# Performance work log

Measured on AMD Instinct MI355X. Metric: run time of the kernel, lower is better.

## Reference

```python
import jax, jax.numpy as jnp
import numpy as np

B, N = 4096, 64
K1, K2, K3 = 32, 16, 8   # ceil(0.5 * n) at each SAGPooling stage
VOCAB, EMB, H = 25, 32, 128
IN = EMB + 2

def _init(k, shape, scale=None):
    if scale is None:
        scale = (2.0 / sum(shape)) ** 0.5
    return (jax.random.normal(k, shape) * scale).astype(jnp.float32)

def setup_inputs() -> dict:
    key = jax.random.key(0)
    ks = jax.random.split(key, 20)
    # band adjacency: residues within sequence distance 2 (peptide backbone graph)
    i = np.arange(N)
    band = ((np.abs(i[:, None] - i[None, :]) <= 2) & (i[:, None] != i[None, :])).astype(np.float32)
    adj = jnp.broadcast_to(jnp.asarray(band), (B, N, N))
    return dict(
        aa=jax.random.randint(ks[0], (B, N), 0, VOCAB),
        pos=jax.random.uniform(ks[1], (B, N, 1), dtype=jnp.float32),
        is_cdr3=(jax.random.uniform(ks[2], (B, N, 1)) < 0.3).astype(jnp.float32),
        adj=adj,
        emb=_init(ks[3], (VOCAB, EMB), 1.0),
        W1=_init(ks[4], (IN, H)), b1=jnp.zeros((H,), jnp.float32),
        p1_wl=_init(ks[5], (H, 1)), p1_bl=jnp.zeros((1,), jnp.float32), p1_wr=_init(ks[6], (H, 1)),
        W2=_init(ks[7], (H, H)), b2=jnp.zeros((H,), jnp.float32),
        p2_wl=_init(ks[8], (H, 1)), p2_bl=jnp.zeros((1,), jnp.float32), p2_wr=_init(ks[9], (H, 1)),
        W3=_init(ks[10], (H, H)), b3=jnp.zeros((H,), jnp.float32),
        p3_wl=_init(ks[11], (H, 1)), p3_bl=jnp.zeros((1,), jnp.float32), p3_wr=_init(ks[12], (H, 1)),
        mW1=_init(ks[13], (2 * H, H)), mb1=jnp.zeros((H,), jnp.float32),
        mW2=_init(ks[14], (H, H // 2)), mb2=jnp.zeros((H // 2,), jnp.float32),
        mW3=_init(ks[15], (H // 2, 1)), mb3=jnp.zeros((1,), jnp.float32),
    )

def _gcn(x, adj, W, b):
    # GCNConv: D^-1/2 (A+I) D^-1/2 (x W) + b
    n = adj.shape[-1]
    a = adj + jnp.eye(n, dtype=adj.dtype)
    dinv = jax.lax.rsqrt(jnp.maximum(a.sum(-1), 1e-12))
    norm = dinv[:, :, None] * a * dinv[:, None, :]
    return jnp.einsum('bij,bjf->bif', norm, x @ W) + b

def _sag_pool(x, adj, wl, bl, wr, k):
    # SAGPooling default GNN is GraphConv: score = W_rel (A x) + b + W_root x
    s = (jnp.einsum('bij,bjf->bif', adj, x) @ wl + bl + x @ wr)[..., 0]  # [B,n]
    vals, idx = jax.lax.top_k(s, k)                                      # per-graph top-k
    xs = jnp.take_along_axis(x, idx[:, :, None], axis=1) * jnp.tanh(vals)[:, :, None]
    a = jnp.take_along_axis(adj, idx[:, :, None], axis=1)                # filter edges to
    a = jnp.take_along_axis(a, idx[:, None, :], axis=2)                  # selected nodes
    return xs, a

def _readout(x):
    # cat([global_max_pool, global_mean_pool]) over nodes of each graph
    return jnp.concatenate([x.max(axis=1), x.mean(axis=1)], axis=-1)

def _forward(pos, is_cdr3, adj, emb, W1, b1, p1_wl, p1_bl, p1_wr, W2, b2, p2_wl, p2_bl, p2_wr, W3, b3, p3_wl, p3_bl, p3_wr, mW1, mb1, mW2, mb2, mW3, mb3, aa):
    x = jnp.concatenate([emb[aa], pos, is_cdr3], axis=-1)   # [B,N,IN]
    x = jax.nn.relu(_gcn(x, adj, W1, b1))
    x, a = _sag_pool(x, adj, p1_wl, p1_bl, p1_wr, K1)
    r = _readout(x)
    x = jax.nn.relu(_gcn(x, a, W2, b2))
    x, a = _sag_pool(x, a, p2_wl, p2_bl, p2_wr, K2)
    r = r + _readout(x)
    x = jax.nn.relu(_gcn(x, a, W3, b3))
    x, a = _sag_pool(x, a, p3_wl, p3_bl, p3_wr, K3)
    r = r + _readout(x)
    h = jax.nn.relu(r @ mW1 + mb1)   # dropout: identity in eval mode
    h = jax.nn.relu(h @ mW2 + mb2)
    return (h @ mW3 + mb3)[:, 0]     # logits [B]

def reference(aa, pos, is_cdr3, adj, emb, W1, b1, p1_wl, p1_bl, p1_wr, W2, b2, p2_wl, p2_bl, p2_wr, W3, b3, p3_wl, p3_bl, p3_wr, mW1, mb1, mW2, mb2, mW3, mb3):
    return _forward(pos, is_cdr3, adj, emb, W1, b1, p1_wl, p1_bl, p1_wr, W2, b2, p2_wl, p2_bl, p2_wr, W3, b3, p3_wl, p3_bl, p3_wr, mW1, mb1, mW2, mb2, mW3, mb3, aa)
```

## Files before the change

### kernel.cpp

```cpp
#include <hip/hip_runtime.h>
#include <math.h>

#define TPB 256
static constexpr int N0 = 64;
static constexpr int H  = 128;
static constexpr int LD = 132;

#define SCHED_FENCE() __builtin_amdgcn_sched_barrier(0)

typedef const __attribute__((address_space(1))) unsigned int glb_u32;
typedef __attribute__((address_space(3))) unsigned int lds_u32;

struct alignas(16) Shm {
  float B[32 * LD];
  float B2[2304];
  float dinvS[32];
  unsigned long long adjS[32];
};

__device__ __forceinline__ unsigned long long& adjPad(float* Bb, int i) {
  return *((unsigned long long*)(Bb + (i >> 1) * LD + 128) + (i & 1));
}

template<int W>
__device__ __forceinline__ float redsum(float v) {
  #pragma unroll
  for (int m = W >> 1; m; m >>= 1) v += __shfl_xor(v, m, 64);
  return v;
}
template<int W>
__device__ __forceinline__ int redsum_i(int v) {
  #pragma unroll
  for (int m = W >> 1; m; m >>= 1) v += __shfl_xor(v, m, 64);
  return v;
}

template<int NN, int GROUPS, int CPT, int STRIDE, bool PADJ>
__device__ __forceinline__ void agg_inplace(float* buf, float* adjb,
    const float* dinv, int tid) {
  float acc[CPT];
  const int i = tid & (NN - 1);
  const int g = tid / NN;
  const bool act = (g < GROUPS);
  if (act) {
    unsigned long long m =
        (PADJ ? adjPad(adjb, i) : ((const unsigned long long*)adjb)[i]) | (1ull << i);
    #pragma unroll
    for (int c = 0; c < CPT; ++c) acc[c] = 0.f;
    const float* base = buf + g * CPT;
    #pragma unroll 1
    while (m) {
      int j = __builtin_ctzll(m); m &= m - 1;
      float a = dinv[j];
      const float* xp = base + j * STRIDE;
      #pragma unroll
      for (int c = 0; c < CPT; c += 4) {
        float4 xv = *(const float4*)(xp + c);
        acc[c]     += a * xv.x; acc[c + 1] += a * xv.y;
        acc[c + 2] += a * xv.z; acc[c + 3] += a * xv.w;
      }
    }
    float di = dinv[i];
    #pragma unroll
    for (int c = 0; c < CPT; ++c) acc[c] *= di;
  }
  __syncthreads();
  if (act) {
    float* op = buf + i * STRIDE + g * CPT;
    #pragma unroll
    for (int c = 0; c < CPT; c += 4)
      *(float4*)(op + c) = make_float4(acc[c], acc[c + 1], acc[c + 2], acc[c + 3]);
  }
  __syncthreads();
  SCHED_FENCE();
}

template<int R, int K, int KREAL, int MODE>
__device__ __forceinline__ void gemm_gw(const float* z, int zld,
    const float* __restrict__ Wg, const float* __restrict__ bg,
    float* out, int old_,
    const float* __restrict__ wl, const float* __restrict__ wr,
    float* uuP, float* svP, const float* tvP, const int* selP, int tid) {
  constexpr int NR = R / 8;
  constexpr int KC = 4;
  const int fc = (tid & 31) * 4;
  const int r0 = (tid >> 5) * NR;
  float4 acc[NR];
  int zoff[NR];
  #pragma unroll
  for (int r = 0; r < NR; ++r) {
    acc[r] = make_float4(0.f, 0.f, 0.f, 0.f);
    int row = (MODE == 2) ? selP[r0 + r] : (r0 + r);
    zoff[r] = row * zld;
  }
  float4 w[KC], nw[KC];
  #pragma unroll
  for (int k = 0; k < KC; ++k)
    w[k] = (k < KREAL) ? *(const float4*)(Wg + k * H + fc)
                       : make_float4(0.f, 0.f, 0.f, 0.f);
  #pragma unroll 1
  for (int kt = 0; kt < K; kt += KC) {
    if (kt + KC < K) {
      #pragma unroll
      for (int k = 0; k < KC; ++k) {
        int gr = kt + KC + k;
        nw[k] = (gr < KREAL) ? *(const float4*)(Wg + gr * H + fc)
                             : make_float4(0.f, 0.f, 0.f, 0.f);
      }
    }
    #pragma unroll
    for (int r = 0; r < NR; ++r) {
      float4 zv = *(const float4*)(z + zoff[r] + kt);
      acc[r].x += zv.x * w[0].x + zv.y * w[1].x + zv.z * w[2].x + zv.w * w[3].x;
      acc[r].y += zv.x * w[0].y + zv.y * w[1].y + zv.z * w[2].y + zv.w * w[3].y;
      acc[r].z += zv.x * w[0].z + zv.y * w[1].z + zv.z * w[2].z + zv.w * w[3].z;
      acc[r].w += zv.x * w[0].w + zv.y * w[1].w + zv.z * w[2].w + zv.w * w[3].w;
    }
    #pragma unroll
    for (int k = 0; k < KC; ++k) w[k] = nw[k];
  }
  const float4 b4 = *(const float4*)(bg + fc);
  if constexpr (MODE == 1) {
    const float4 wl4 = *(const float4*)(wl + fc);
    const float4 wr4 = *(const float4*)(wr + fc);
    #pragma unroll
    for (int r = 0; r < NR; ++r) {
      float y0 = fmaxf(acc[r].x + b4.x, 0.f);
      float y1 = fmaxf(acc[r].y + b4.y, 0.f);
      float y2 = fmaxf(acc[r].z + b4.z, 0.f);
      float y3 = fmaxf(acc[r].w + b4.w, 0.f);
      float up = y0 * wl4.x + y1 * wl4.y + y2 * wl4.z + y3 * wl4.w;
      float vp = y0 * wr4.x + y1 * wr4.y + y2 * wr4.z + y3 * wr4.w;
      up = redsum<32>(up);
      vp = redsum<32>(vp);
      if ((tid & 31) == 0) { uuP[r0 + r] = up; svP[r0 + r] = vp; }
    }
  } else {
    #pragma unroll
    for (int r = 0; r < NR; ++r) {
      float t = (MODE == 2) ? tvP[r0 + r] : 1.f;
      float4 o;
      o.x = fmaxf(acc[r].x + b4.x, 0.f) * t;
      o.y = fmaxf(acc[r].y + b4.y, 0.f) * t;
      o.z = fmaxf(acc[r].z + b4.z, 0.f) * t;
      o.w = fmaxf(acc[r].w + b4.w, 0.f) * t;
      *(float4*)(out + (r0 + r) * old_ + fc) = o;
    }
  }
}

__device__ __forceinline__ void stage_w8(const float* gsrc, float* ldst,
                                         int wv, int ln) {
  __builtin_amdgcn_global_load_lds(
      (glb_u32*)(gsrc + wv * 256 + ln * 4),
      (lds_u32*)(ldst + wv * 256),
      16, 0, 0);
}

template<int R>
__device__ __forceinline__ void gemm128_lds(float* zb,
    float* wt0, float* wt1,
    const float* __restrict__ Wg, const float* __restrict__ bg, int tid) {
  constexpr int NR = R / 8;
  const int fc = (tid & 31) * 4;
  const int r0 = (tid >> 5) * NR;
  const int wv = tid >> 6;
  const int ln = tid & 63;
  float4 acc[NR];
  int zoff[NR];
  #pragma unroll
  for (int r = 0; r < NR; ++r) {
    acc[r] = make_float4(0.f, 0.f, 0.f, 0.f);
    zoff[r] = (r0 + r) * LD;
  }
  stage_w8(Wg, wt0, wv, ln);
  asm volatile("s_waitcnt vmcnt(0)" ::: "memory");
  __syncthreads();
  #pragma unroll 1
  for (int kt = 0; kt < 128; kt += 8) {
    const int t = kt >> 3;
    const float* cur = (t & 1) ? wt1 : wt0;
    float* nxt = (t & 1) ? wt0 : wt1;
    if (kt + 8 < 128) stage_w8(Wg + (kt + 8) * H, nxt, wv, ln);
    #pragma unroll
    for (int kc = 0; kc < 8; kc += 4) {
      float4 w0 = *(const float4*)(cur + (kc + 0) * H + fc);
      float4 w1 = *(const float4*)(cur + (kc + 1) * H + fc);
      float4 w2 = *(const float4*)(cur + (kc + 2) * H + fc);
      float4 w3 = *(const float4*)(cur + (kc + 3) * H + fc);
      #pragma unroll
      for (int r = 0; r < NR; ++r) {
        float4 zv = *(const float4*)(zb + zoff[r] + kt + kc);
        acc[r].x += zv.x * w0.x + zv.y * w1.x + zv.z * w2.x + zv.w * w3.x;
        acc[r].y += zv.x * w0.y + zv.y * w1.y + zv.z * w2.y + zv.w * w3.y;
        acc[r].z += zv.x * w0.z + zv.y * w1.z + zv.z * w2.z + zv.w * w3.z;
        acc[r].w += zv.x * w0.w + zv.y * w1.w + zv.z * w2.w + zv.w * w3.w;
      }
    }
    asm volatile("s_waitcnt vmcnt(0)" ::: "memory");
    __syncthreads();
  }
  const float4 b4 = *(const float4*)(bg + fc);
  #pragma unroll
  for (int r = 0; r < NR; ++r) {
    float4 o;
    o.x = fmaxf(acc[r].x + b4.x, 0.f);
    o.y = fmaxf(acc[r].y + b4.y, 0.f);
    o.z = fmaxf(acc[r].z + b4.z, 0.f);
    o.w = fmaxf(acc[r].w + b4.w, 0.f);
    *(float4*)(zb + zoff[r] + fc) = o;
  }
}

template<int NN, bool PADJ>
__device__ __forceinline__ void score(float* adjb, const float* uu, float* sv,
                                      float bl, int tid) {
  if (tid < NN) {
    unsigned long long m =
        PADJ ? adjPad(adjb, tid) : ((const unsigned long long*)adjb)[tid];
    float a = bl + sv[tid];
    #pragma unroll 1
    while (m) { int j = __builtin_ctzll(m); m &= m - 1; a += uu[j]; }
    sv[tid] = a;
  }
}

template<int NN, int KK, int RKP>
__device__ __forceinline__ void rank_topk(const float* sv, float* tv, int* sel,
                                          int tid) {
  int i = tid / RKP, p = tid % RKP;
  constexpr int CHr = NN / RKP;
  float si = sv[i];
  int cnt = 0;
  #pragma unroll
  for (int c = 0; c < CHr; ++c) {
    int j = p * CHr + c;
    float sj = sv[j];
    cnt += (sj > si || (sj == si && j < i)) ? 1 : 0;
  }
  cnt = redsum_i<RKP>(cnt);
  if (p == 0 && cnt < KK) { sel[cnt] = i; tv[cnt] = tanhf(si); }
}

template<int KK>
__device__ __forceinline__ void readout(const float* xn, int ld, int tid,
                                        float& rm, float& rs) {
  if (tid < H) {
    float m = -INFINITY, s = 0.f;
    #pragma unroll
    for (int r = 0; r < KK; ++r) {
      float v = xn[r * ld + tid];
      m = fmaxf(m, v); s += v;
    }
    rm += m;
    rs += s * (1.f / KK);
  }
}

template<int NN, int KK, int UVP, int RKP, bool DOFILT>
__device__ __forceinline__ void sag_pool_inplace(Shm& sh, float* x,
    const float* __restrict__ wl, const float* __restrict__ blp,
    const float* __restrict__ wr,
    float* uu, float* sv, float* tv, int* sel, int tid, float& rm, float& rs) {
  {
    int dot = tid / UVP, p = tid % UVP;
    int j = dot >> 1;
    const float* wp = (dot & 1) ? wr : wl;
    constexpr int CH = H / UVP;
    const float* xr = x + j * LD + p * CH;
    const float* wq = wp + p * CH;
    float a = 0.f;
    #pragma unroll
    for (int k = 0; k < CH; k += 4) {
      float4 xv = *(const float4*)(xr + k);
      float4 wv = *(const float4*)(wq + k);
      a += xv.x * wv.x + xv.y * wv.y + xv.z * wv.z + xv.w * wv.w;
    }
    a = redsum<UVP>(a);
    if (p == 0) { if (dot & 1) sv[j] = a; else uu[j] = a; }
  }
  __syncthreads();
  SCHED_FENCE();
  score<NN, false>((float*)sh.adjS, uu, sv, blp[0], tid);
  __syncthreads();
  rank_topk<NN, KK, RKP>(sv, tv, sel, tid);
  __syncthreads();
  SCHED_FENCE();
  unsigned long long oldrow = 0ull;
  if (tid < KK) oldrow = sh.adjS[sel[tid]];
  constexpr int NV  = KK * (H / 4);
  constexpr int PER = (NV + TPB - 1) / TPB;
  float4 stg[PER]; int dst[PER];
  #pragma unroll
  for (int q = 0; q < PER; ++q) {
    int e = tid + q * TPB;
    if (e < NV) {
      int r = e / (H / 4), c = (e % (H / 4)) * 4;
      float4 v = *(const float4*)(x + sel[r] * LD + c);
      float t = tv[r];
      stg[q] = make_float4(v.x * t, v.y * t, v.z * t, v.w * t);
      dst[q] = r * LD + c;
    }
  }
  __syncthreads();
  #pragma unroll
  for (int q = 0; q < PER; ++q) {
    int e = tid + q * TPB;
    if (e < NV) *(float4*)(x + dst[q]) = stg[q];
  }
  __syncthreads();
  SCHED_FENCE();
  if (DOFILT && tid < KK) {
    unsigned long long nm = 0ull;
    #pragma unroll 1
    for (int c = 0; c < KK; ++c)
      nm |= ((oldrow >> sel[c]) & 1ull) << c;
    sh.adjS[tid] = nm;
    sh.dinvS[tid] = rsqrtf(1.f + (float)__popcll(nm));
  }
  readout<KK>(x, LD, tid, rm, rs);
  __syncthreads();
  SCHED_FENCE();
}

__global__ __launch_bounds__(TPB, 5) void sagpool_fused(
    const int* __restrict__ aa, const float* __restrict__ pos,
    const float* __restrict__ cdr, const float* __restrict__ adjG,
    const float* __restrict__ emb,
    const float* __restrict__ W1, const float* __restrict__ b1,
    const float* __restrict__ p1wl, const float* __restrict__ p1bl, const float* __restrict__ p1wr,
    const float* __restrict__ W2, const float* __restrict__ b2,
    const float* __restrict__ p2wl, const float* __restrict__ p2bl, const float* __restrict__ p2wr,
    const float* __restrict__ W3, const float* __restrict__ b3,
    const float* __restrict__ p3wl, const float* __restrict__ p3bl, const float* __restrict__ p3wr,
    const float* __restrict__ mW1, const float* __restrict__ mb1,
    const float* __restrict__ mW2, const float* __restrict__ mb2,
    const float* __restrict__ mW3, const float* __restrict__ mb3,
    float* __restrict__ out)
{
  __shared__ Shm sh;
  const int b   = blockIdx.x;
  const int tid = threadIdx.x;

  float* dinv64 = (float*)sh.adjS;
  float* tv1    = (float*)sh.adjS;
  int*   sel1   = (int*)sh.adjS + 32;
  float* uu1 = sh.B;        float* sv1 = sh.B + 64;
  float* uu23 = sh.B2;      float* sv23 = sh.B2 + 64;
  float* tv23 = sh.B2 + 128; int* sel23 = (int*)(sh.B2 + 160);

  float rm = 0.f, rs = 0.f;

  {
    const float* rp = adjG + (size_t)b * (N0 * N0) + (tid >> 2) * N0 + (tid & 3) * 16;
    unsigned long long mpart = 0ull;
    #pragma unroll
    for (int q = 0; q < 16; q += 4) {
      float4 v = *(const float4*)(rp + q);
      unsigned int bits = (v.x != 0.f ? 1u : 0u) | (v.y != 0.f ? 2u : 0u)
                        | (v.z != 0.f ? 4u : 0u) | (v.w != 0.f ? 8u : 0u);
      mpart |= (unsigned long long)bits << q;
    }
    mpart <<= ((tid & 3) * 16);
    mpart |= __shfl_xor(mpart, 1, 64);
    mpart |= __shfl_xor(mpart, 2, 64);
    if ((tid & 3) == 0) {
      int r = tid >> 2;
      adjPad(sh.B, r) = mpart;
      dinv64[r] = rsqrtf(1.f + (float)__popcll(mpart));
    }
  }
  SCHED_FENCE();
  #pragma unroll 1
  for (int e = tid; e < N0 * 36; e += TPB) {
    int j = e / 36, k = e - j * 36;
    int node = b * N0 + j;
    float v;
    if (k < 32)       v = emb[aa[node] * 32 + k];
    else if (k == 32) v = pos[node];
    else if (k == 33) v = cdr[node];
    else              v = 0.f;
    sh.B2[e] = v;
  }
  __syncthreads();
  SCHED_FENCE();

  agg_inplace<64, 3, 12, 36, true>(sh.B2, sh.B, dinv64, tid);
  gemm_gw<64, 36, 34, 1>(sh.B2, 36, W1, b1, nullptr, 0, p1wl, p1wr,
                         uu1, sv1, nullptr, nullptr, tid);
  __syncthreads();
  SCHED_FENCE();
  score<64, true>(sh.B, uu1, sv1, p1bl[0], tid);
  __syncthreads();
  rank_topk<64, 32, 4>(sv1, tv1, sel1, tid);
  __syncthreads();
  SCHED_FENCE();
  gemm_gw<32, 36, 34, 2>(sh.B2, 36, W1, b1, sh.B, LD, nullptr, nullptr,
                         nullptr, nullptr, tv1, sel1, tid);
  __syncthreads();
  SCHED_FENCE();
  if (tid < 32) {
    unsigned long long oldrow = adjPad(sh.B, sel1[tid]);
    unsigned long long nm = 0ull;
    #pragma unroll 1
    for (int c = 0; c < 32; ++c)
      nm |= ((oldrow >> sel1[c]) & 1ull) << c;
    sh.adjS[tid] = nm;
    sh.dinvS[tid] = rsqrtf(1.f + (float)__popcll(nm));
  }
  readout<32>(sh.B, LD, tid, rm, rs);
  __syncthreads();
  SCHED_FENCE();

  agg_inplace<32, 8, 16, LD, false>(sh.B, (float*)sh.adjS, sh.dinvS, tid);
  gemm128_lds<32>(sh.B, sh.B2, sh.B2 + 1024, W2, b2, tid);
  __syncthreads();
  SCHED_FENCE();
  sag_pool_inplace<32, 16, 4, 8, true>(sh, sh.B, p2wl, p2bl, p2wr,
                                       uu23, sv23, tv23, sel23, tid, rm, rs);

  agg_inplace<16, 16, 8, LD, false>(sh.B, (float*)sh.adjS, sh.dinvS, tid);
  gemm128_lds<16>(sh.B, sh.B2, sh.B2 + 1024, W3, b3, tid);
  __syncthreads();
  SCHED_FENCE();
  sag_pool_inplace<16, 8, 8, 16, false>(sh, sh.B, p3wl, p3bl, p3wr,
                                        uu23, sv23, tv23, sel23, tid, rm, rs);

  if (tid < H) { sh.B2[tid] = rm; sh.B2[H + tid] = rs; }
  __syncthreads();
  SCHED_FENCE();
  {
    int f = tid & (H - 1), p = tid >> 7;
    const int base = p * 128;
    float a = 0.f;
    #pragma unroll 4
    for (int k = 0; k < 128; ++k) a += sh.B2[base + k] * mW1[(base + k) * H + f];
    sh.B2[384 + p * H + f] = a;
  }
  __syncthreads();
  SCHED_FENCE();
  if (tid < H) {
    float a = mb1[tid] + sh.B2[384 + tid] + sh.B2[384 + H + tid];
    sh.B2[256 + tid] = fmaxf(a, 0.f);
  }
  __syncthreads();
  SCHED_FENCE();
  {
    int o = tid & 63, p = tid >> 6;
    const int base = p * 32;
    float a = 0.f;
    #pragma unroll 4
    for (int k = 0; k < 32; ++k) a += sh.B2[256 + base + k] * mW2[(base + k) * 64 + o];
    sh.B2[640 + p * 64 + o] = a;
  }
  __syncthreads();
  SCHED_FENCE();
  if (tid < 64) {
    float a = sh.B2[640 + tid] + sh.B2[704 + tid] + sh.B2[768 + tid] + sh.B2[832 + tid];
    a = fmaxf(a + mb2[tid], 0.f);
    float v = a * mW3[tid];
    v = redsum<64>(v);
    if (tid == 0) out[b] = v + mb3[0];
  }
}

extern "C" void kernel_launch(void* const* d_in, const int* in_sizes, int n_in,
                              void* d_out, int out_size, void* d_ws, size_t ws_size,
                              hipStream_t stream) {
  (void)n_in; (void)d_ws; (void)ws_size; (void)out_size;
  const int*   aa   = (const int*)  d_in[0];
  const float* pos  = (const float*)d_in[1];
  const float* cdr  = (const float*)d_in[2];
  const float* adj  = (const float*)d_in[3];
  const float* emb  = (const float*)d_in[4];
  const float* W1   = (const float*)d_in[5];
  const float* b1   = (const float*)d_in[6];
  const float* p1wl = (const float*)d_in[7];
  const float* p1bl = (const float*)d_in[8];
  const float* p1wr = (const float*)d_in[9];
  const float* W2   = (const float*)d_in[10];
  const float* b2   = (const float*)d_in[11];
  const float* p2wl = (const float*)d_in[12];
  const float* p2bl = (const float*)d_in[13];
  const float* p2wr = (const float*)d_in[14];
  const float* W3   = (const float*)d_in[15];
  const float* b3   = (const float*)d_in[16];
  const float* p3wl = (const float*)d_in[17];
  const float* p3bl = (const float*)d_in[18];
  const float* p3wr = (const float*)d_in[19];
  const float* mW1  = (const float*)d_in[20];
  const float* mb1  = (const float*)d_in[21];
  const float* mW2  = (const float*)d_in[22];
  const float* mb2  = (const float*)d_in[23];
  const float* mW3  = (const float*)d_in[24];
  const float* mb3  = (const float*)d_in[25];
  float* out = (float*)d_out;

  const int B = in_sizes[0] / N0;
  hipLaunchKernelGGL(sagpool_fused, dim3(B), dim3(TPB), 0, stream,
                     aa, pos, cdr, adj, emb,
                     W1, b1, p1wl, p1bl, p1wr,
                     W2, b2, p2wl, p2bl, p2wr,
                     W3, b3, p3wl, p3bl, p3wr,
                     mW1, mb1, mW2, mb2, mW3, mb3, out);
}
```

Before: 245.0 us.

## Keep GEMM outputs in registers, fuse score dot products, scatter only selected rows

The GEMM epilogues now keep the ReLU output in registers and compute the SAGPooling score dot products (wl, wr) with warp reductions. After top-k ranking, each node's rank is recorded and only the selected rows are written to shared memory, scaled by tanh. This removes the stage-1 recompute GEMM over the selected rows, the separate score dot-product pass, and the staged gather/copy in sag_pool. It costs extra live registers for the held accumulators, which at launch bounds of 5 blocks could raise register pressure.

```diff
diff --git a/kernel.cpp b/kernel.cpp
--- a/kernel.cpp
+++ b/kernel.cpp
@@ -75,24 +75,17 @@
   SCHED_FENCE();
 }
 
-template<int R, int K, int KREAL, int MODE>
-__device__ __forceinline__ void gemm_gw(const float* z, int zld,
+template<int R, int K, int KREAL>
+__device__ __forceinline__ void gemm_s1_uv(const float* z, int zld,
     const float* __restrict__ Wg, const float* __restrict__ bg,
-    float* out, int old_,
     const float* __restrict__ wl, const float* __restrict__ wr,
-    float* uuP, float* svP, const float* tvP, const int* selP, int tid) {
+    float* uuP, float* svP, float4* acc, int tid) {
   constexpr int NR = R / 8;
   constexpr int KC = 4;
   const int fc = (tid & 31) * 4;
   const int r0 = (tid >> 5) * NR;
-  float4 acc[NR];
-  int zoff[NR];
-  #pragma unroll
-  for (int r = 0; r < NR; ++r) {
-    acc[r] = make_float4(0.f, 0.f, 0.f, 0.f);
-    int row = (MODE == 2) ? selP[r0 + r] : (r0 + r);
-    zoff[r] = row * zld;
-  }
+  #pragma unroll
+  for (int r = 0; r < NR; ++r) acc[r] = make_float4(0.f, 0.f, 0.f, 0.f);
   float4 w[KC], nw[KC];
   #pragma unroll
   for (int k = 0; k < KC; ++k)
@@ -110,7 +103,7 @@
     }
     #pragma unroll
     for (int r = 0; r < NR; ++r) {
-      float4 zv = *(const float4*)(z + zoff[r] + kt);
+      float4 zv = *(const float4*)(z + (r0 + r) * zld + kt);
       acc[r].x += zv.x * w[0].x + zv.y * w[1].x + zv.z * w[2].x + zv.w * w[3].x;
       acc[r].y += zv.x * w[0].y + zv.y * w[1].y + zv.z * w[2].y + zv.w * w[3].y;
       acc[r].z += zv.x * w[0].z + zv.y * w[1].z + zv.z * w[2].z + zv.w * w[3].z;
@@ -119,33 +112,22 @@
     #pragma unroll
     for (int k = 0; k < KC; ++k) w[k] = nw[k];
   }
-  const float4 b4 = *(const float4*)(bg + fc);
-  if constexpr (MODE == 1) {
-    const float4 wl4 = *(const float4*)(wl + fc);
-    const float4 wr4 = *(const float4*)(wr + fc);
-    #pragma unroll
-    for (int r = 0; r < NR; ++r) {
-      float y0 = fmaxf(acc[r].x + b4.x, 0.f);
-      float y1 = fmaxf(acc[r].y + b4.y, 0.f);
-      float y2 = fmaxf(acc[r].z + b4.z, 0.f);
-      float y3 = fmaxf(acc[r].w + b4.w, 0.f);
-      float up = y0 * wl4.x + y1 * wl4.y + y2 * wl4.z + y3 * wl4.w;
-      float vp = y0 * wr4.x + y1 * wr4.y + y2 * wr4.z + y3 * wr4.w;
-      up = redsum<32>(up);
-      vp = redsum<32>(vp);
-      if ((tid & 31) == 0) { uuP[r0 + r] = up; svP[r0 + r] = vp; }
-    }
-  } else {
-    #pragma unroll
-    for (int r = 0; r < NR; ++r) {
-      float t = (MODE == 2) ? tvP[r0 + r] : 1.f;
-      float4 o;
-      o.x = fmaxf(acc[r].x + b4.x, 0.f) * t;
-      o.y = fmaxf(acc[r].y + b4.y, 0.f) * t;
-      o.z = fmaxf(acc[r].z + b4.z, 0.f) * t;
-      o.w = fmaxf(acc[r].w + b4.w, 0.f) * t;
-      *(float4*)(out + (r0 + r) * old_ + fc) = o;
-    }
+  const float4 b4  = *(const float4*)(bg + fc);
+  const float4 wl4 = *(const float4*)(wl + fc);
+  const float4 wr4 = *(const float4*)(wr + fc);
+  #pragma unroll
+  for (int r = 0; r < NR; ++r) {
+    float4 y;
+    y.x = fmaxf(acc[r].x + b4.x, 0.f);
+    y.y = fmaxf(acc[r].y + b4.y, 0.f);
+    y.z = fmaxf(acc[r].z + b4.z, 0.f);
+    y.w = fmaxf(acc[r].w + b4.w, 0.f);
+    acc[r] = y;
+    float up = y.x * wl4.x + y.y * wl4.y + y.z * wl4.z + y.w * wl4.w;
+    float vp = y.x * wr4.x + y.y * wr4.y + y.z * wr4.z + y.w * wr4.w;
+    up = redsum<32>(up);
+    vp = redsum<32>(vp);
+    if ((tid & 31) == 0) { uuP[r0 + r] = up; svP[r0 + r] = vp; }
   }
 }
 
@@ -158,21 +140,18 @@
 }
 
 template<int R>
-__device__ __forceinline__ void gemm128_lds(float* zb,
+__device__ __forceinline__ void gemm128_uv(const float* zb,
     float* wt0, float* wt1,
-    const float* __restrict__ Wg, const float* __restrict__ bg, int tid) {
+    const float* __restrict__ Wg, const float* __restrict__ bg,
+    const float* __restrict__ wl, const float* __restrict__ wr,
+    float* uuP, float* svP, float4* acc, int tid) {
   constexpr int NR = R / 8;
   const int fc = (tid & 31) * 4;
   const int r0 = (tid >> 5) * NR;
   const int wv = tid >> 6;
   const int ln = tid & 63;
-  float4 acc[NR];
-  int zoff[NR];
-  #pragma unroll
-  for (int r = 0; r < NR; ++r) {
-    acc[r] = make_float4(0.f, 0.f, 0.f, 0.f);
-    zoff[r] = (r0 + r) * LD;
-  }
+  #pragma unroll
+  for (int r = 0; r < NR; ++r) acc[r] = make_float4(0.f, 0.f, 0.f, 0.f);
   stage_w8(Wg, wt0, wv, ln);
   asm volatile("s_waitcnt vmcnt(0)" ::: "memory");
   __syncthreads();
@@ -190,7 +169,7 @@
       float4 w3 = *(const float4*)(cur + (kc + 3) * H + fc);
       #pragma unroll
       for (int r = 0; r < NR; ++r) {
-        float4 zv = *(const float4*)(zb + zoff[r] + kt + kc);
+        float4 zv = *(const float4*)(zb + (r0 + r) * LD + kt + kc);
         acc[r].x += zv.x * w0.x + zv.y * w1.x + zv.z * w2.x + zv.w * w3.x;
         acc[r].y += zv.x * w0.y + zv.y * w1.y + zv.z * w2.y + zv.w * w3.y;
         acc[r].z += zv.x * w0.z + zv.y * w1.z + zv.z * w2.z + zv.w * w3.z;
@@ -200,15 +179,22 @@
     asm volatile("s_waitcnt vmcnt(0)" ::: "memory");
     __syncthreads();
   }
-  const float4 b4 = *(const float4*)(bg + fc);
+  const float4 b4  = *(const float4*)(bg + fc);
+  const float4 wl4 = *(const float4*)(wl + fc);
+  const float4 wr4 = *(const float4*)(wr + fc);
   #pragma unroll
   for (int r = 0; r < NR; ++r) {
-    float4 o;
-    o.x = fmaxf(acc[r].x + b4.x, 0.f);
-    o.y = fmaxf(acc[r].y + b4.y, 0.f);
-    o.z = fmaxf(acc[r].z + b4.z, 0.f);
-    o.w = fmaxf(acc[r].w + b4.w, 0.f);
-    *(float4*)(zb + zoff[r] + fc) = o;
+    float4 y;
+    y.x = fmaxf(acc[r].x + b4.x, 0.f);
+    y.y = fmaxf(acc[r].y + b4.y, 0.f);
+    y.z = fmaxf(acc[r].z + b4.z, 0.f);
+    y.w = fmaxf(acc[r].w + b4.w, 0.f);
+    acc[r] = y;
+    float up = y.x * wl4.x + y.y * wl4.y + y.z * wl4.z + y.w * wl4.w;
+    float vp = y.x * wr4.x + y.y * wr4.y + y.z * wr4.z + y.w * wr4.w;
+    up = redsum<32>(up);
+    vp = redsum<32>(vp);
+    if ((tid & 31) == 0) { uuP[r0 + r] = up; svP[r0 + r] = vp; }
   }
 }
 
@@ -226,8 +212,8 @@
 }
 
 template<int NN, int KK, int RKP>
-__device__ __forceinline__ void rank_topk(const float* sv, float* tv, int* sel,
-                                          int tid) {
+__device__ __forceinline__ void rank_topk_rk(const float* sv, float* tv,
+    int* sel, int* rkOf, int tid) {
   int i = tid / RKP, p = tid % RKP;
   constexpr int CHr = NN / RKP;
   float si = sv[i];
@@ -239,7 +225,26 @@
     cnt += (sj > si || (sj == si && j < i)) ? 1 : 0;
   }
   cnt = redsum_i<RKP>(cnt);
-  if (p == 0 && cnt < KK) { sel[cnt] = i; tv[cnt] = tanhf(si); }
+  if (p == 0) {
+    if (cnt < KK) { sel[cnt] = i; tv[cnt] = tanhf(si); }
+    rkOf[i] = (cnt < KK) ? cnt : -1;
+  }
+}
+
+template<int NR>
+__device__ __forceinline__ void cond_write(const float4* acc, const float* tv,
+    const int* rkOf, float* out, int tid) {
+  const int fc = (tid & 31) * 4;
+  const int r0 = (tid >> 5) * NR;
+  #pragma unroll
+  for (int r = 0; r < NR; ++r) {
+    int rk = rkOf[r0 + r];
+    if (rk >= 0) {
+      float t = tv[rk];
+      *(float4*)(out + rk * LD + fc) =
+          make_float4(acc[r].x * t, acc[r].y * t, acc[r].z * t, acc[r].w * t);
+    }
+  }
 }
 
 template<int KK>
@@ -255,72 +260,6 @@
     rm += m;
     rs += s * (1.f / KK);
   }
-}
-
-template<int NN, int KK, int UVP, int RKP, bool DOFILT>
-__device__ __forceinline__ void sag_pool_inplace(Shm& sh, float* x,
-    const float* __restrict__ wl, const float* __restrict__ blp,
-    const float* __restrict__ wr,
-    float* uu, float* sv, float* tv, int* sel, int tid, float& rm, float& rs) {
-  {
-    int dot = tid / UVP, p = tid % UVP;
-    int j = dot >> 1;
-    const float* wp = (dot & 1) ? wr : wl;
-    constexpr int CH = H / UVP;
-    const float* xr = x + j * LD + p * CH;
-    const float* wq = wp + p * CH;
-    float a = 0.f;
-    #pragma unroll
-    for (int k = 0; k < CH; k += 4) {
-      float4 xv = *(const float4*)(xr + k);
-      float4 wv = *(const float4*)(wq + k);
-      a += xv.x * wv.x + xv.y * wv.y + xv.z * wv.z + xv.w * wv.w;
-    }
-    a = redsum<UVP>(a);
-    if (p == 0) { if (dot & 1) sv[j] = a; else uu[j] = a; }
-  }
-  __syncthreads();
-  SCHED_FENCE();
-  score<NN, false>((float*)sh.adjS, uu, sv, blp[0], tid);
-  __syncthreads();
-  rank_topk<NN, KK, RKP>(sv, tv, sel, tid);
-  __syncthreads();
-  SCHED_FENCE();
-  unsigned long long oldrow = 0ull;
-  if (tid < KK) oldrow = sh.adjS[sel[tid]];
-  constexpr int NV  = KK * (H / 4);
-  constexpr int PER = (NV + TPB - 1) / TPB;
-  float4 stg[PER]; int dst[PER];
-  #pragma unroll
-  for (int q = 0; q < PER; ++q) {
-    int e = tid + q * TPB;
-    if (e < NV) {
-      int r = e / (H / 4), c = (e % (H / 4)) * 4;
-      float4 v = *(const float4*)(x + sel[r] * LD + c);
-      float t = tv[r];
-      stg[q] = make_float4(v.x * t, v.y * t, v.z * t, v.w * t);
-      dst[q] = r * LD + c;
-    }
-  }
-  __syncthreads();
-  #pragma unroll
-  for (int q = 0; q < PER; ++q) {
-    int e = tid + q * TPB;
-    if (e < NV) *(float4*)(x + dst[q]) = stg[q];
-  }
-  __syncthreads();
-  SCHED_FENCE();
-  if (DOFILT && tid < KK) {
-    unsigned long long nm = 0ull;
-    #pragma unroll 1
-    for (int c = 0; c < KK; ++c)
-      nm |= ((oldrow >> sel[c]) & 1ull) << c;
-    sh.adjS[tid] = nm;
-    sh.dinvS[tid] = rsqrtf(1.f + (float)__popcll(nm));
-  }
-  readout<KK>(x, LD, tid, rm, rs);
-  __syncthreads();
-  SCHED_FENCE();
 }
 
 __global__ __launch_bounds__(TPB, 5) void sagpool_fused(
@@ -345,9 +284,11 @@
   float* dinv64 = (float*)sh.adjS;
   float* tv1    = (float*)sh.adjS;
   int*   sel1   = (int*)sh.adjS + 32;
-  float* uu1 = sh.B;        float* sv1 = sh.B + 64;
+  float* uu1 = sh.B;       float* sv1 = sh.B + 64;
+  int*   rkOf1 = (int*)sh.B2;
   float* uu23 = sh.B2;      float* sv23 = sh.B2 + 64;
   float* tv23 = sh.B2 + 128; int* sel23 = (int*)(sh.B2 + 160);
+  int*   rkOf23 = (int*)(sh.B2 + 192);
 
   float rm = 0.f, rs = 0.f;
 
@@ -386,17 +327,16 @@
   SCHED_FENCE();
 
   agg_inplace<64, 3, 12, 36, true>(sh.B2, sh.B, dinv64, tid);
-  gemm_gw<64, 36, 34, 1>(sh.B2, 36, W1, b1, nullptr, 0, p1wl, p1wr,
-                         uu1, sv1, nullptr, nullptr, tid);
+  float4 y1[8];
+  gemm_s1_uv<64, 36, 34>(sh.B2, 36, W1, b1, p1wl, p1wr, uu1, sv1, y1, tid);
   __syncthreads();
   SCHED_FENCE();
   score<64, true>(sh.B, uu1, sv1, p1bl[0], tid);
   __syncthreads();
-  rank_topk<64, 32, 4>(sv1, tv1, sel1, tid);
-  __syncthreads();
-  SCHED_FENCE();
-  gemm_gw<32, 36, 34, 2>(sh.B2, 36, W1, b1, sh.B, LD, nullptr, nullptr,
-                         nullptr, nullptr, tv1, sel1, tid);
+  rank_topk_rk<64, 32, 4>(sv1, tv1, sel1, rkOf1, tid);
+  __syncthreads();
+  SCHED_FENCE();
+  cond_write<8>(y1, tv1, rkOf1, sh.B, tid);
   __syncthreads();
   SCHED_FENCE();
   if (tid < 32) {
@@ -413,18 +353,49 @@
   SCHED_FENCE();
 
   agg_inplace<32, 8, 16, LD, false>(sh.B, (float*)sh.adjS, sh.dinvS, tid);
-  gemm128_lds<32>(sh.B, sh.B2, sh.B2 + 1024, W2, b2, tid);
-  __syncthreads();
-  SCHED_FENCE();
-  sag_pool_inplace<32, 16, 4, 8, true>(sh, sh.B, p2wl, p2bl, p2wr,
-                                       uu23, sv23, tv23, sel23, tid, rm, rs);
+  float4 y2[4];
+  gemm128_uv<32>(sh.B, sh.B2, sh.B2 + 1024, W2, b2, p2wl, p2wr,
+                 uu23, sv23, y2, tid);
+  __syncthreads();
+  SCHED_FENCE();
+  score<32, false>((float*)sh.adjS, uu23, sv23, p2bl[0], tid);
+  __syncthreads();
+  rank_topk_rk<32, 16, 8>(sv23, tv23, sel23, rkOf23, tid);
+  __syncthreads();
+  SCHED_FENCE();
+  cond_write<4>(y2, tv23, rkOf23, sh.B, tid);
+  if (tid < 16) {
+    unsigned long long oldrow = sh.adjS[sel23[tid]];
+    unsigned long long nm = 0ull;
+    #pragma unroll 1
+    for (int c = 0; c < 16; ++c)
+      nm |= ((oldrow >> sel23[c]) & 1ull) << c;
+    sh.adjS[tid] = nm;
+    sh.dinvS[tid] = rsqrtf(1.f + (float)__popcll(nm));
+  }
+  __syncthreads();
+  SCHED_FENCE();
+  readout<16>(sh.B, LD, tid, rm, rs);
+  __syncthreads();
+  SCHED_FENCE();
 
   agg_inplace<16, 16, 8, LD, false>(sh.B, (float*)sh.adjS, sh.dinvS, tid);
-  gemm128_lds<16>(sh.B, sh.B2, sh.B2 + 1024, W3, b3, tid);
-  __syncthreads();
-  SCHED_FENCE();
-  sag_pool_inplace<16, 8, 8, 16, false>(sh, sh.B, p3wl, p3bl, p3wr,
-                                        uu23, sv23, tv23, sel23, tid, rm, rs);
+  float4 y3[2];
+  gemm128_uv<16>(sh.B, sh.B2, sh.B2 + 1024, W3, b3, p3wl, p3wr,
+                 uu23, sv23, y3, tid);
+  __syncthreads();
+  SCHED_FENCE();
+  score<16, false>((float*)sh.adjS, uu23, sv23, p3bl[0], tid);
+  __syncthreads();
+  rank_topk_rk<16, 8, 16>(sv23, tv23, sel23, rkOf23, tid);
+  __syncthreads();
+  SCHED_FENCE();
+  cond_write<2>(y3, tv23, rkOf23, sh.B, tid);
+  __syncthreads();
+  SCHED_FENCE();
+  readout<8>(sh.B, LD, tid, rm, rs);
+  __syncthreads();
+  SCHED_FENCE();
 
   if (tid < H) { sh.B2[tid] = rm; sh.B2[H + tid] = rs; }
   __syncthreads();
```

After: 221.6 us. 1.11x faster.
